# Performance work log

Hardware: AMD Instinct MI355X
Metric: run time of the kernel (lower is better)

## Reference

```python
import jax, jax.numpy as jnp
import numpy as np

# config (mirrors init_kwargs)
H = 768        # hidden_size
NH = 12        # n_heads
HD = H // NH   # head_size = 64 (rotary 'per_head' dim)
INTER = 3072   # intermediate_size
NL = 6         # n_layers
V = 32768      # vocab_size
AW = 256       # attention_width
SEQLEN = 512   # packed per-sequence length (batch['length'])
B = 16         # number of packed sequences
N = B * SEQLEN # total tokens


def _layer_norm(x, scale, offset, eps=1e-5):
    m = jnp.mean(x, axis=-1, keepdims=True)
    var = jnp.mean(jnp.square(x - m), axis=-1, keepdims=True)
    return (x - m) * jax.lax.rsqrt(var + eps) * scale + offset


def _rotate_every_two(x):
    x1 = x[..., ::2]
    x2 = x[..., 1::2]
    return jnp.stack((-x2, x1), axis=-1).reshape(x.shape)


def _fixed_pos_embedding(ages, dim):
    # ages: [N] float32 -> sin, cos: [N, dim]
    inv_freq = 1.0 / 10000 ** jnp.linspace(0.0, 2.0, num=dim // 2)
    t = ages[:, None] * inv_freq[None, :]          # [N, dim//2]
    s, c = jnp.sin(t), jnp.cos(t)
    sin = jnp.stack((s, s), axis=-1).reshape(ages.shape[0], dim)
    cos = jnp.stack((c, c), axis=-1).reshape(ages.shape[0], dim)
    return sin, cos


def _local_attention(q, k, v, seg_len, width):
    # q,k,v: [NH, N, HD]. Causal attention within a sliding window of `width`,
    # restricted to segments of size seg_len (the (i & ~(length-1)) mask in piton).
    nh, n, hd = q.shape
    b = n // seg_len
    qb = q.reshape(nh, b, seg_len, hd)
    kb = k.reshape(nh, b, seg_len, hd)
    vb = v.reshape(nh, b, seg_len, hd)
    scale = jnp.asarray(1.0 / np.sqrt(hd), q.dtype)
    scores = jnp.einsum('hbqd,hbkd->hbqk', qb, kb) * scale
    i = jnp.arange(seg_len)[:, None]
    j = jnp.arange(seg_len)[None, :]
    mask = (j <= i) & (i - j < width)
    scores = jnp.where(mask, scores, jnp.asarray(-1e30, scores.dtype))
    probs = jax.nn.softmax(scores, axis=-1)
    out = jnp.einsum('hbqk,hbkd->hbqd', probs, vb)
    return out.reshape(nh, n, hd)


def _block(x, sin, cos, seg_len, p):
    scale, offset, w_in, b_in, w_out, b_out = p
    xn = _layer_norm(x, scale, offset)
    mid = xn @ w_in + b_in                               # fused QKV + FF proj
    q, k, v, ff = jnp.split(mid, [H, 2 * H, 3 * H], axis=-1)

    def to_heads(t):  # [N, H] -> [NH, N, HD]
        return t.reshape(t.shape[0], NH, HD).transpose(1, 0, 2)

    q, k, v = to_heads(q), to_heads(k), to_heads(v)
    # rotary == 'per_head': applied after head split, sin/cos broadcast over heads
    q = q * cos[None] + _rotate_every_two(q) * sin[None]
    k = k * cos[None] + _rotate_every_two(k) * sin[None]
    attn = _local_attention(q, k, v, seg_len, AW)
    shaped = attn.transpose(1, 0, 2).reshape(x.shape)    # [N, H]
    combined = jnp.concatenate((shaped, jax.nn.gelu(ff)), axis=-1)
    # NOTE: original returns normed-x + output_proj(combined) (x was reassigned)
    return xn + combined @ w_out + b_out


def setup_inputs() -> dict:
    key = jax.random.key(0)
    ks = jax.random.split(key, 8)
    return {
        'tokens': jax.random.randint(ks[0], (N,), 0, V, dtype=jnp.int32),
        'ages': jax.random.uniform(ks[1], (N,), jnp.float32, 0.0, 10000.0),
        'normalized_ages': jax.random.normal(ks[2], (N,), jnp.float32),
        'length': SEQLEN,
        'embed': jax.random.normal(ks[3], (V, H), jnp.float32) / np.sqrt(H),
        'ln_scale': jnp.ones((NL, H), jnp.float32),
        'ln_offset': jnp.zeros((NL, H), jnp.float32),
        'w_in': jax.random.normal(ks[4], (NL, H, 3 * H + INTER), jnp.float32) / np.sqrt(H),
        'b_in': jnp.zeros((NL, 3 * H + INTER), jnp.float32),
        'w_out': jax.random.normal(ks[5], (NL, H + INTER, H), jnp.float32) * (2.0 / (NL * np.sqrt(H))),
        'b_out': jnp.zeros((NL, H), jnp.float32),
        'final_scale': jnp.ones((H,), jnp.float32),
        'final_offset': jnp.zeros((H,), jnp.float32),
    }


def reference(tokens, ages, normalized_ages, length, embed, ln_scale, ln_offset,
              w_in, b_in, w_out, b_out, final_scale, final_offset):
    x = embed[tokens]                                  # [N, H]
    sin, cos = _fixed_pos_embedding(ages, HD)          # rotary == 'per_head'

    def step(carry, p):
        return _block(carry, sin, cos, length, p), None

    x, _ = jax.lax.scan(step, x, (ln_scale, ln_offset, w_in, b_in, w_out, b_out))
    return _layer_norm(x, final_scale, final_offset)
```

## Files before the change

### kernel.cpp

```cpp
#include <hip/hip_runtime.h>
#include <hip/hip_bf16.h>

#define H_    768
#define NH_   12
#define HD_   64
#define INTER_ 3072
#define NL_   6
#define NTOK  8192
#define SEG   512
#define NB    16
#define AW_   256
#define MIDW  5376
#define CMB   3840

typedef unsigned short u16;
typedef __bf16 bf16;
typedef bf16  bf16x8 __attribute__((ext_vector_type(8)));
typedef float f32x4  __attribute__((ext_vector_type(4)));
typedef u16   u16x8  __attribute__((ext_vector_type(8)));

__device__ __forceinline__ u16 f2bf(float f) {
    union { float f; unsigned u; } v; v.f = f;
    unsigned u = v.u;
    u += 0x7fffu + ((u >> 16) & 1u);
    return (u16)(u >> 16);
}
__device__ __forceinline__ float bf2f(u16 h) {
    union { unsigned u; float f; } v; v.u = ((unsigned)h) << 16; return v.f;
}
__device__ __forceinline__ float gelu_f(float x) {
    float x3 = x * x * x;
    return 0.5f * x * (1.f + tanhf(0.7978845608028654f * (x + 0.044715f * x3)));
}

__global__ void k_embed(const int* __restrict__ tokens, const float* __restrict__ embed,
                        float* __restrict__ x) {
    int row = blockIdx.x;
    int tok = tokens[row];
    const float* src = embed + (size_t)tok * H_;
    float* dst = x + (size_t)row * H_;
    for (int c = threadIdx.x; c < H_; c += blockDim.x) dst[c] = src[c];
}

__global__ void k_tables(const float* __restrict__ ages, float* __restrict__ st,
                         float* __restrict__ ct) {
    int n = blockIdx.x * blockDim.x + threadIdx.x;
    if (n >= NTOK) return;
    float age = ages[n];
    for (int j = 0; j < 32; j++) {
        float e = (float)j * (2.0f / 31.0f);
        float invf = 1.0f / powf(10000.0f, e);
        float t = age * invf;
        st[n * 32 + j] = sinf(t);
        ct[n * 32 + j] = cosf(t);
    }
}

__global__ void k_transpose_bf16(const float* __restrict__ src, u16* __restrict__ dst,
                                 int R, int C) {
    __shared__ float T[64][65];
    int l = blockIdx.z;
    const float* s = src + (size_t)l * R * C;
    u16* d = dst + (size_t)l * R * C;
    int r0 = blockIdx.y * 64, c0 = blockIdx.x * 64;
    for (int i = threadIdx.x; i < 64 * 64; i += blockDim.x) {
        int r = i >> 6, c = i & 63;
        T[r][c] = s[(size_t)(r0 + r) * C + c0 + c];
    }
    __syncthreads();
    for (int i = threadIdx.x; i < 64 * 64; i += blockDim.x) {
        int rr = i >> 6, cc = i & 63;
        d[(size_t)(c0 + rr) * R + r0 + cc] = f2bf(T[cc][rr]);
    }
}

template<int FINAL>
__global__ __launch_bounds__(256) void k_ln(const float* __restrict__ x,
        const float* __restrict__ scale, const float* __restrict__ offset,
        float* __restrict__ xn_f, u16* __restrict__ xn_h, float* __restrict__ outf) {
    int wid = threadIdx.x >> 6, lane = threadIdx.x & 63;
    int row = blockIdx.x * 4 + wid;
    const float* xr = x + (size_t)row * H_;
    float4 v[3];
    float s = 0.f, sq = 0.f;
#pragma unroll
    for (int i = 0; i < 3; i++) {
        v[i] = *(const float4*)&xr[(i * 64 + lane) * 4];
        s  += v[i].x + v[i].y + v[i].z + v[i].w;
        sq += v[i].x * v[i].x + v[i].y * v[i].y + v[i].z * v[i].z + v[i].w * v[i].w;
    }
    for (int m = 1; m < 64; m <<= 1) { s += __shfl_xor(s, m); sq += __shfl_xor(sq, m); }
    float mean = s * (1.f / 768.f);
    float var  = sq * (1.f / 768.f) - mean * mean;
    float rstd = rsqrtf(fmaxf(var, 0.f) + 1e-5f);
#pragma unroll
    for (int i = 0; i < 3; i++) {
        int c0 = (i * 64 + lane) * 4;
        float4 sc = *(const float4*)&scale[c0];
        float4 of = *(const float4*)&offset[c0];
        float y0 = (v[i].x - mean) * rstd * sc.x + of.x;
        float y1 = (v[i].y - mean) * rstd * sc.y + of.y;
        float y2 = (v[i].z - mean) * rstd * sc.z + of.z;
        float y3 = (v[i].w - mean) * rstd * sc.w + of.w;
        if (FINAL) {
            *(float4*)&outf[(size_t)row * H_ + c0] = make_float4(y0, y1, y2, y3);
        } else {
            *(float4*)&xn_f[(size_t)row * H_ + c0] = make_float4(y0, y1, y2, y3);
            ushort4 h = make_ushort4(f2bf(y0), f2bf(y1), f2bf(y2), f2bf(y3));
            *(ushort4*)&xn_h[(size_t)row * H_ + c0] = h;
        }
    }
}

template<int MODE>
__global__ __launch_bounds__(256) void k_gemm(
        const u16* __restrict__ A, const u16* __restrict__ A2,
        const u16* __restrict__ Bt, const float* __restrict__ bias,
        const float* __restrict__ xn_f, u16* __restrict__ Cmid,
        float* __restrict__ Xout, int Ksz) {
    __shared__ u16 As[128 * 72];
    __shared__ u16 Bs[128 * 72];
    int m0 = blockIdx.x * 128;
    int n0 = blockIdx.y * 128;
    int tid = threadIdx.x;
    int wid = tid >> 6, lane = tid & 63;
    int wm = wid >> 1, wn = wid & 1;
    f32x4 acc[4][4] = {};

    int nkt = Ksz / 64;
    for (int kt = 0; kt < nkt; kt++) {
        int k0 = kt * 64;
        const u16* Ap; int lda, acol;
        if (MODE == 2 && k0 >= H_) { Ap = A2; lda = MIDW; acol = 2304 + (k0 - H_); }
        else                       { Ap = A;  lda = H_;   acol = k0; }
#pragma unroll
        for (int i = 0; i < 4; i++) {
            int q = i * 256 + tid;
            int r = q >> 3, c8 = q & 7;
            uint4 d = *(const uint4*)&Ap[(size_t)(m0 + r) * lda + acol + c8 * 8];
            *(uint4*)&As[r * 72 + c8 * 8] = d;
        }
#pragma unroll
        for (int i = 0; i < 4; i++) {
            int q = i * 256 + tid;
            int r = q >> 3, c8 = q & 7;
            uint4 d = *(const uint4*)&Bt[(size_t)(n0 + r) * Ksz + k0 + c8 * 8];
            *(uint4*)&Bs[r * 72 + c8 * 8] = d;
        }
        __syncthreads();
#pragma unroll
        for (int kk = 0; kk < 64; kk += 32) {
            bf16x8 af[4], bfr[4];
#pragma unroll
            for (int mi = 0; mi < 4; mi++)
                af[mi] = *(const bf16x8*)&As[(wm * 64 + mi * 16 + (lane & 15)) * 72 + kk + (lane >> 4) * 8];
#pragma unroll
            for (int ni = 0; ni < 4; ni++)
                bfr[ni] = *(const bf16x8*)&Bs[(wn * 64 + ni * 16 + (lane & 15)) * 72 + kk + (lane >> 4) * 8];
#pragma unroll
            for (int mi = 0; mi < 4; mi++)
#pragma unroll
                for (int ni = 0; ni < 4; ni++)
                    acc[mi][ni] = __builtin_amdgcn_mfma_f32_16x16x32_bf16(af[mi], bfr[ni], acc[mi][ni], 0, 0, 0);
        }
        __syncthreads();
    }
    int rbase = m0 + wm * 64, cbase = n0 + wn * 64;
#pragma unroll
    for (int mi = 0; mi < 4; mi++) {
#pragma unroll
        for (int ni = 0; ni < 4; ni++) {
            int col = cbase + ni * 16 + (lane & 15);
            float b = bias[col];
#pragma unroll
            for (int r = 0; r < 4; r++) {
                int row = rbase + mi * 16 + (lane >> 4) * 4 + r;
                float vv = acc[mi][ni][r] + b;
                if (MODE == 1) {
                    if (col >= 2304) vv = gelu_f(vv);
                    Cmid[(size_t)row * MIDW + col] = f2bf(vv);
                } else {
                    Xout[(size_t)row * H_ + col] = vv + xn_f[(size_t)row * H_ + col];
                }
            }
        }
    }
}

__global__ __launch_bounds__(256) void k_rope_v(u16* __restrict__ mid,
        const float* __restrict__ st, const float* __restrict__ ct, u16* __restrict__ Vt) {
    int nb = blockIdx.x, h = blockIdx.y;
    int n0 = nb * 64;
    __shared__ u16 Vl[64][72];
    int tid = threadIdx.x;
    for (int i = tid; i < 64 * 32; i += 256) {
        int r = i >> 5, j = i & 31;
        int n = n0 + r;
        float s = st[n * 32 + j], c = ct[n * 32 + j];
        size_t base = (size_t)n * MIDW + h * 64 + 2 * j;
        float q0 = bf2f(mid[base]), q1 = bf2f(mid[base + 1]);
        mid[base]     = f2bf(q0 * c - q1 * s);
        mid[base + 1] = f2bf(q1 * c + q0 * s);
        float k0 = bf2f(mid[base + H_]), k1 = bf2f(mid[base + H_ + 1]);
        mid[base + H_]     = f2bf(k0 * c - k1 * s);
        mid[base + H_ + 1] = f2bf(k1 * c + k0 * s);
    }
    for (int i = tid; i < 64 * 64; i += 256) {
        int r = i >> 6, d = i & 63;
        Vl[r][d] = mid[(size_t)(n0 + r) * MIDW + 1536 + h * 64 + d];
    }
    __syncthreads();
    for (int i = tid; i < 64 * 64; i += 256) {
        int d = i >> 6, r = i & 63;
        Vt[(size_t)(h * 64 + d) * NTOK + n0 + r] = Vl[r][d];
    }
}

__global__ __launch_bounds__(128) void k_attn(const u16* __restrict__ mid,
        const u16* __restrict__ Vt, u16* __restrict__ attn_out) {
    int bx = blockIdx.x;
    int h = bx >> 8, rem = bx & 255, b = rem >> 4, qq = rem & 15;
    int t0 = (qq * 32 - 255) >> 6; if (t0 < 0) t0 = 0;
    int tend = qq >> 1;
    int nt = tend - t0 + 1;
    int tid = threadIdx.x, wid = tid >> 6, lane = tid & 63;
    __shared__ float S[32][324];
    __shared__ float rl[32];
    int qrow0 = b * SEG + qq * 32;

    bf16x8 qf[2];
    {
        int r = qrow0 + wid * 16 + (lane & 15);
        const u16* qp = &mid[(size_t)r * MIDW + h * 64];
        qf[0] = *(const bf16x8*)&qp[(lane >> 4) * 8];
        qf[1] = *(const bf16x8*)&qp[32 + (lane >> 4) * 8];
    }
    for (int t = 0; t < nt; t++) {
        int j0 = (t0 + t) * 64;
        f32x4 sa[4] = {};
#pragma unroll
        for (int kf = 0; kf < 2; kf++) {
            bf16x8 kfr[4];
#pragma unroll
            for (int nf = 0; nf < 4; nf++) {
                int key = b * SEG + j0 + nf * 16 + (lane & 15);
                kfr[nf] = *(const bf16x8*)&mid[(size_t)key * MIDW + H_ + h * 64 + kf * 32 + (lane >> 4) * 8];
            }
#pragma unroll
            for (int nf = 0; nf < 4; nf++)
                sa[nf] = __builtin_amdgcn_mfma_f32_16x16x32_bf16(qf[kf], kfr[nf], sa[nf], 0, 0, 0);
        }
#pragma unroll
        for (int nf = 0; nf < 4; nf++) {
            int j = j0 + nf * 16 + (lane & 15);
#pragma unroll
            for (int r = 0; r < 4; r++) {
                int row = wid * 16 + (lane >> 4) * 4 + r;
                int qi = qq * 32 + row;
                bool valid = (j <= qi) && (qi - j < AW_);
                S[row][t * 64 + nf * 16 + (lane & 15)] = valid ? sa[nf][r] * 0.125f : -1e30f;
            }
        }
    }
    __syncthreads();
    {
        int row = tid >> 2, sub = tid & 3;
        int ncol = nt * 64;
        float m = -1e30f;
        for (int c = sub; c < ncol; c += 4) m = fmaxf(m, S[row][c]);
        m = fmaxf(m, __shfl_xor(m, 1)); m = fmaxf(m, __shfl_xor(m, 2));
        float l = 0.f;
        for (int c = sub; c < ncol; c += 4) { float p = __expf(S[row][c] - m); S[row][c] = p; l += p; }
        l += __shfl_xor(l, 1); l += __shfl_xor(l, 2);
        if (sub == 0) rl[row] = 1.f / l;
    }
    __syncthreads();
    f32x4 oacc[4] = {};
    for (int t = 0; t < nt; t++) {
#pragma unroll
        for (int kf = 0; kf < 2; kf++) {
            const float* sp = &S[wid * 16 + (lane & 15)][t * 64 + kf * 32 + (lane >> 4) * 8];
            float4 f1 = *(const float4*)sp;
            float4 f2 = *(const float4*)(sp + 4);
            u16x8 pt;
            pt[0] = f2bf(f1.x); pt[1] = f2bf(f1.y); pt[2] = f2bf(f1.z); pt[3] = f2bf(f1.w);
            pt[4] = f2bf(f2.x); pt[5] = f2bf(f2.y); pt[6] = f2bf(f2.z); pt[7] = f2bf(f2.w);
            bf16x8 pa = __builtin_bit_cast(bf16x8, pt);
#pragma unroll
            for (int nf = 0; nf < 4; nf++) {
                int d = h * 64 + nf * 16 + (lane & 15);
                const u16* vp = &Vt[(size_t)d * NTOK + b * SEG + (t0 + t) * 64 + kf * 32 + (lane >> 4) * 8];
                bf16x8 vb = *(const bf16x8*)vp;
                oacc[nf] = __builtin_amdgcn_mfma_f32_16x16x32_bf16(pa, vb, oacc[nf], 0, 0, 0);
            }
        }
    }
#pragma unroll
    for (int nf = 0; nf < 4; nf++) {
#pragma unroll
        for (int r = 0; r < 4; r++) {
            int row = wid * 16 + (lane >> 4) * 4 + r;
            float sc = rl[row];
            int grow = qrow0 + row;
            attn_out[(size_t)grow * H_ + h * 64 + nf * 16 + (lane & 15)] = f2bf(oacc[nf][r] * sc);
        }
    }
}

extern "C" void kernel_launch(void* const* d_in, const int* in_sizes, int n_in,
                              void* d_out, int out_size, void* d_ws, size_t ws_size,
                              hipStream_t stream) {
    const int*   tokens   = (const int*)d_in[0];
    const float* ages     = (const float*)d_in[1];
    const float* embed    = (const float*)d_in[4];
    const float* ln_scale = (const float*)d_in[5];
    const float* ln_off   = (const float*)d_in[6];
    const float* w_in     = (const float*)d_in[7];
    const float* b_in     = (const float*)d_in[8];
    const float* w_out    = (const float*)d_in[9];
    const float* b_out    = (const float*)d_in[10];
    const float* fscale   = (const float*)d_in[11];
    const float* foff     = (const float*)d_in[12];
    float* out = (float*)d_out;

    char* ws = (char*)d_ws;
    size_t off = 0;
    auto alloc = [&](size_t bytes) { void* p = ws + off; off += (bytes + 255) & ~(size_t)255; return p; };
    float* st      = (float*)alloc((size_t)NTOK * 32 * 4);
    float* ct      = (float*)alloc((size_t)NTOK * 32 * 4);
    float* x       = (float*)alloc((size_t)NTOK * H_ * 4);
    float* xn_f    = (float*)alloc((size_t)NTOK * H_ * 4);
    u16*   xn_h    = (u16*)alloc((size_t)NTOK * H_ * 2);
    u16*   mid     = (u16*)alloc((size_t)NTOK * MIDW * 2);
    u16*   Vt      = (u16*)alloc((size_t)H_ * NTOK * 2);
    u16*   attn    = (u16*)alloc((size_t)NTOK * H_ * 2);
    u16*   w_in_t  = (u16*)alloc((size_t)NL_ * H_ * MIDW * 2);
    u16*   w_out_t = (u16*)alloc((size_t)NL_ * CMB * H_ * 2);

    k_embed<<<NTOK, 256, 0, stream>>>(tokens, embed, x);
    k_tables<<<(NTOK + 255) / 256, 256, 0, stream>>>(ages, st, ct);
    k_transpose_bf16<<<dim3(MIDW / 64, H_ / 64, NL_), 256, 0, stream>>>(w_in, w_in_t, H_, MIDW);
    k_transpose_bf16<<<dim3(H_ / 64, CMB / 64, NL_), 256, 0, stream>>>(w_out, w_out_t, CMB, H_);

    for (int l = 0; l < NL_; l++) {
        k_ln<0><<<NTOK / 4, 256, 0, stream>>>(x, ln_scale + l * H_, ln_off + l * H_, xn_f, xn_h, nullptr);
        k_gemm<1><<<dim3(NTOK / 128, MIDW / 128), 256, 0, stream>>>(
            xn_h, nullptr, w_in_t + (size_t)l * H_ * MIDW, b_in + (size_t)l * MIDW,
            nullptr, mid, nullptr, H_);
        k_rope_v<<<dim3(NTOK / 64, NH_), 256, 0, stream>>>(mid, st, ct, Vt);
        k_attn<<<NH_ * NB * 16, 128, 0, stream>>>(mid, Vt, attn);
        k_gemm<2><<<dim3(NTOK / 128, H_ / 128), 256, 0, stream>>>(
            attn, mid, w_out_t + (size_t)l * CMB * H_, b_out + (size_t)l * H_,
            xn_f, nullptr, x, CMB);
    }
    k_ln<1><<<NTOK / 4, 256, 0, stream>>>(x, fscale, foff, nullptr, nullptr, out);
}
```

Measured before the change: 2.468 ms.

## Load GEMM tiles directly into LDS and use narrower tiles for output projection

The GEMM kernel now fills its shared-memory tiles with global_load_lds, which copies global memory straight into LDS instead of staging each tile through registers. The tiles are stored unpadded with a row stride of 64, because each wave must write one contiguous 1 KB block. The kernel is templated on tile width, and the output projection switches to 128x64 tiles with a 4x1 wave layout, doubling its block count to fill more compute units. The cost is that unpadded LDS rows may cause bank conflicts when fragments are read for the MFMA instructions, and the narrower tile reuses each A tile less.

After: 2.495 ms. About the same (+1.1%).

```diff
diff --git a/kernel.cpp b/kernel.cpp
--- a/kernel.cpp
+++ b/kernel.cpp
@@ -18,6 +18,10 @@
 typedef bf16  bf16x8 __attribute__((ext_vector_type(8)));
 typedef float f32x4  __attribute__((ext_vector_type(4)));
 typedef u16   u16x8  __attribute__((ext_vector_type(8)));
+
+#define GLOAD16(gp, lp) \
+    __builtin_amdgcn_global_load_lds((const __attribute__((address_space(1))) void*)(gp), \
+                                     (__attribute__((address_space(3))) void*)(lp), 16, 0, 0)
 
 __device__ __forceinline__ u16 f2bf(float f) {
     union { float f; unsigned u; } v; v.f = f;
@@ -112,20 +116,27 @@
     }
 }
 
-template<int MODE>
+template<int MODE, int BN>
 __global__ __launch_bounds__(256) void k_gemm(
         const u16* __restrict__ A, const u16* __restrict__ A2,
         const u16* __restrict__ Bt, const float* __restrict__ bias,
         const float* __restrict__ xn_f, u16* __restrict__ Cmid,
         float* __restrict__ Xout, int Ksz) {
-    __shared__ u16 As[128 * 72];
-    __shared__ u16 Bs[128 * 72];
+    __shared__ __align__(16) u16 As[128 * 64];
+    __shared__ __align__(16) u16 Bs[BN * 64];
     int m0 = blockIdx.x * 128;
-    int n0 = blockIdx.y * 128;
+    int n0 = blockIdx.y * BN;
     int tid = threadIdx.x;
     int wid = tid >> 6, lane = tid & 63;
-    int wm = wid >> 1, wn = wid & 1;
-    f32x4 acc[4][4] = {};
+    constexpr int MI = (BN == 128) ? 4 : 2;
+    constexpr int NI = 4;
+    int wm = (BN == 128) ? (wid >> 1) : wid;
+    int wn = (BN == 128) ? (wid & 1) : 0;
+    f32x4 acc[MI][NI] = {};
+
+    int r = tid >> 3;
+    int c = (tid & 7) * 8;
+    int wbase = (tid & 192) * 8;
 
     int nkt = Ksz / 64;
     for (int kt = 0; kt < nkt; kt++) {
@@ -134,48 +145,40 @@
         if (MODE == 2 && k0 >= H_) { Ap = A2; lda = MIDW; acol = 2304 + (k0 - H_); }
         else                       { Ap = A;  lda = H_;   acol = k0; }
 #pragma unroll
-        for (int i = 0; i < 4; i++) {
-            int q = i * 256 + tid;
-            int r = q >> 3, c8 = q & 7;
-            uint4 d = *(const uint4*)&Ap[(size_t)(m0 + r) * lda + acol + c8 * 8];
-            *(uint4*)&As[r * 72 + c8 * 8] = d;
-        }
-#pragma unroll
-        for (int i = 0; i < 4; i++) {
-            int q = i * 256 + tid;
-            int r = q >> 3, c8 = q & 7;
-            uint4 d = *(const uint4*)&Bt[(size_t)(n0 + r) * Ksz + k0 + c8 * 8];
-            *(uint4*)&Bs[r * 72 + c8 * 8] = d;
-        }
+        for (int i = 0; i < 4; i++)
+            GLOAD16(&Ap[(size_t)(m0 + i * 32 + r) * lda + acol + c], &As[i * 2048 + wbase]);
+#pragma unroll
+        for (int i = 0; i < BN / 32; i++)
+            GLOAD16(&Bt[(size_t)(n0 + i * 32 + r) * Ksz + k0 + c], &Bs[i * 2048 + wbase]);
         __syncthreads();
 #pragma unroll
         for (int kk = 0; kk < 64; kk += 32) {
-            bf16x8 af[4], bfr[4];
-#pragma unroll
-            for (int mi = 0; mi < 4; mi++)
-                af[mi] = *(const bf16x8*)&As[(wm * 64 + mi * 16 + (lane & 15)) * 72 + kk + (lane >> 4) * 8];
-#pragma unroll
-            for (int ni = 0; ni < 4; ni++)
-                bfr[ni] = *(const bf16x8*)&Bs[(wn * 64 + ni * 16 + (lane & 15)) * 72 + kk + (lane >> 4) * 8];
-#pragma unroll
-            for (int mi = 0; mi < 4; mi++)
-#pragma unroll
-                for (int ni = 0; ni < 4; ni++)
+            bf16x8 af[MI], bfr[NI];
+#pragma unroll
+            for (int mi = 0; mi < MI; mi++)
+                af[mi] = *(const bf16x8*)&As[(wm * (MI * 16) + mi * 16 + (lane & 15)) * 64 + kk + (lane >> 4) * 8];
+#pragma unroll
+            for (int ni = 0; ni < NI; ni++)
+                bfr[ni] = *(const bf16x8*)&Bs[(wn * 64 + ni * 16 + (lane & 15)) * 64 + kk + (lane >> 4) * 8];
+#pragma unroll
+            for (int mi = 0; mi < MI; mi++)
+#pragma unroll
+                for (int ni = 0; ni < NI; ni++)
                     acc[mi][ni] = __builtin_amdgcn_mfma_f32_16x16x32_bf16(af[mi], bfr[ni], acc[mi][ni], 0, 0, 0);
         }
         __syncthreads();
     }
-    int rbase = m0 + wm * 64, cbase = n0 + wn * 64;
-#pragma unroll
-    for (int mi = 0; mi < 4; mi++) {
-#pragma unroll
-        for (int ni = 0; ni < 4; ni++) {
+    int rbase = m0 + wm * (MI * 16), cbase = n0 + wn * 64;
+#pragma unroll
+    for (int mi = 0; mi < MI; mi++) {
+#pragma unroll
+        for (int ni = 0; ni < NI; ni++) {
             int col = cbase + ni * 16 + (lane & 15);
             float b = bias[col];
 #pragma unroll
-            for (int r = 0; r < 4; r++) {
-                int row = rbase + mi * 16 + (lane >> 4) * 4 + r;
-                float vv = acc[mi][ni][r] + b;
+            for (int rr = 0; rr < 4; rr++) {
+                int row = rbase + mi * 16 + (lane >> 4) * 4 + rr;
+                float vv = acc[mi][ni][rr] + b;
                 if (MODE == 1) {
                     if (col >= 2304) vv = gelu_f(vv);
                     Cmid[(size_t)row * MIDW + col] = f2bf(vv);
@@ -344,12 +347,12 @@
 
     for (int l = 0; l < NL_; l++) {
         k_ln<0><<<NTOK / 4, 256, 0, stream>>>(x, ln_scale + l * H_, ln_off + l * H_, xn_f, xn_h, nullptr);
-        k_gemm<1><<<dim3(NTOK / 128, MIDW / 128), 256, 0, stream>>>(
+        k_gemm<1, 128><<<dim3(NTOK / 128, MIDW / 128), 256, 0, stream>>>(
             xn_h, nullptr, w_in_t + (size_t)l * H_ * MIDW, b_in + (size_t)l * MIDW,
             nullptr, mid, nullptr, H_);
         k_rope_v<<<dim3(NTOK / 64, NH_), 256, 0, stream>>>(mid, st, ct, Vt);
         k_attn<<<NH_ * NB * 16, 128, 0, stream>>>(mid, Vt, attn);
-        k_gemm<2><<<dim3(NTOK / 128, H_ / 128), 256, 0, stream>>>(
+        k_gemm<2, 64><<<dim3(NTOK / 128, H_ / 64), 256, 0, stream>>>(
             attn, mid, w_out_t + (size_t)l * CMB * H_, b_out + (size_t)l * H_,
             xn_f, nullptr, x, CMB);
     }
```
